# Performance work log

Hardware: AMD Instinct MI355X
Metric: run time of the kernel (lower is better)

Reference implementation:

```python
import jax, jax.numpy as jnp
import numpy as np
from jax import lax

B, C, H, W, K = 32, 128, 56, 56, 5
CR = C // 4          # reduced channels in weight-gen MLP
CE = 4 * C           # expanded channels
EPS = 1e-6


def setup_inputs() -> dict:
    key = jax.random.key(0)
    ks = jax.random.split(key, 8)
    s = lambda fan: 1.0 / np.sqrt(fan)
    return {
        "x": jax.random.normal(ks[0], (B, C, H, W), jnp.float32),
        "w_fc1": jax.random.normal(ks[1], (CR, C), jnp.float32) * s(C),
        "ln1_w": jnp.ones((CR,), jnp.float32),
        "ln1_b": jnp.zeros((CR,), jnp.float32),
        "w_fc2": jax.random.normal(ks[2], (C * K * K, CR), jnp.float32) * s(CR),
        "ln2_w": jnp.ones((C,), jnp.float32),
        "ln2_b": jnp.zeros((C,), jnp.float32),
        "w_expand": jax.random.normal(ks[3], (CE, C), jnp.float32) * s(C),
        "w_shrink": jax.random.normal(ks[4], (C, CE), jnp.float32) * s(CE),
        "grn_gamma": jax.random.normal(ks[5], (CE,), jnp.float32) * 0.1,
        "grn_beta": jax.random.normal(ks[6], (CE,), jnp.float32) * 0.1,
    }


def _ln(v, w, b, axis):
    u = v.mean(axis, keepdims=True)
    s2 = jnp.square(v - u).mean(axis, keepdims=True)
    return (v - u) * lax.rsqrt(s2 + EPS) * w + b


def reference(x, w_fc1, ln1_w, ln1_b, w_fc2, ln2_w, ln2_b, w_expand, w_shrink,
              grn_gamma, grn_beta):
    b, c, h, w = x.shape
    # ---- dynamic weight generation: pool -> fc1 -> LN -> fc2 ----
    pooled = x.mean((2, 3))                                  # [B, C]
    hdn = pooled @ w_fc1.T                                   # [B, CR]
    hdn = _ln(hdn, ln1_w, ln1_b, axis=-1)                    # channels_first LN over CR
    dyn = hdn @ w_fc2.T                                      # [B, C*K*K]
    dyn_w = dyn.reshape(b * c, 1, K, K)                      # per-sample depthwise kernels
    # ---- per-sample dynamic depthwise conv (groups = B*C) ----
    pad = K // 2
    out = lax.conv_general_dilated(
        x.reshape(1, b * c, h, w), dyn_w,
        window_strides=(1, 1), padding=[(pad, pad), (pad, pad)],
        dimension_numbers=("NCHW", "OIHW", "NCHW"),
        feature_group_count=b * c,
    ).reshape(b, c, h, w)
    # ---- LN (channels_first) over channel dim ----
    u = out.mean(1, keepdims=True)
    s2 = jnp.square(out - u).mean(1, keepdims=True)
    out = (out - u) * lax.rsqrt(s2 + EPS)
    out = ln2_w[None, :, None, None] * out + ln2_b[None, :, None, None]
    # ---- expand 1x1 -> GELU -> GRN -> shrink 1x1 ----
    out = jnp.einsum("bchw,oc->bohw", out, w_expand)         # [B, 4C, H, W]
    out = jax.nn.gelu(out, approximate=False)
    gx = jnp.sqrt(jnp.sum(jnp.square(out), axis=(2, 3), keepdims=True))  # [B,4C,1,1]
    nx = gx / (gx.mean(1, keepdims=True) + EPS)
    g = grn_gamma[None, :, None, None]
    bt = grn_beta[None, :, None, None]
    out = g * (out * nx) + bt + out
    out = jnp.einsum("bohw,co->bchw", out, w_shrink)         # [B, C, H, W]
    return out + x
```

## Files before the change

### kernel.cpp

```cpp
#include <hip/hip_runtime.h>
#include <hip/hip_bf16.h>

#define B_   32
#define C_   128
#define H_   56
#define W_   56
#define HW_  (H_*W_)
#define BHW_ (B_*HW_)
#define K5_  5
#define KK_  25
#define CR_  32
#define CE_  512
#define EPS_ 1e-6f

typedef __hip_bfloat16 bf16;
typedef __attribute__((ext_vector_type(8))) short short8;
typedef __attribute__((ext_vector_type(4))) float f32x4;


__device__ __forceinline__ float wave_reduce_sum(float v) {
#pragma unroll
  for (int off = 32; off > 0; off >>= 1) v += __shfl_down(v, off, 64);
  return v;
}
__device__ __forceinline__ float bf2f(unsigned short u) {
  return __uint_as_float(((unsigned)u) << 16);
}
__device__ __forceinline__ unsigned short f2bf_bits(float f) {
  bf16 h = __float2bfloat16(f);
  unsigned short u;
  __builtin_memcpy(&u, &h, 2);
  return u;
}
__device__ __forceinline__ float fast_gelu(float v) {
  float t = __expf(-1.702f * v);
  return v * __builtin_amdgcn_rcpf(1.0f + t);
}
__device__ __forceinline__ void glds16(const void* g, void* l) {
  __builtin_amdgcn_global_load_lds(
      (const __attribute__((address_space(1))) unsigned int*)g,
      (__attribute__((address_space(3))) unsigned int*)l, 16, 0, 0);
}

__global__ __launch_bounds__(256) void prep_kernel(const float* __restrict__ we,
                                                   const float* __restrict__ ws,
                                                   bf16* __restrict__ weB,
                                                   bf16* __restrict__ wsB,
                                                   float* __restrict__ gx2) {
  int i = blockIdx.x * 256 + threadIdx.x;
  if (i < CE_ * C_)          weB[i] = __float2bfloat16(we[i]);
  else if (i < 2 * CE_ * C_) wsB[i - CE_ * C_] = __float2bfloat16(ws[i - CE_ * C_]);
  else                       gx2[i - 2 * CE_ * C_] = 0.f;
}

__global__ __launch_bounds__(256) void pool_kernel(const float* __restrict__ x,
                                                   float* __restrict__ pooled) {
  int bc = blockIdx.x;
  const float4* xp4 = reinterpret_cast<const float4*>(x + (size_t)bc * HW_);
  float s = 0.f;
  for (int i = threadIdx.x; i < 784; i += 256) {
    float4 v = xp4[i];
    s += (v.x + v.y) + (v.z + v.w);
  }
  s = wave_reduce_sum(s);
  __shared__ float red[4];
  int lane = threadIdx.x & 63, wid = threadIdx.x >> 6;
  if (lane == 0) red[wid] = s;
  __syncthreads();
  if (threadIdx.x == 0) pooled[bc] = (red[0] + red[1] + red[2] + red[3]) * (1.0f / HW_);
}

__global__ __launch_bounds__(256) void fc_kernel(const float* __restrict__ pooled,
                                                 const float* __restrict__ w_fc1,
                                                 const float* __restrict__ ln1_w,
                                                 const float* __restrict__ ln1_b,
                                                 const float* __restrict__ w_fc2,
                                                 float* __restrict__ dyn) {
  int b = blockIdx.x;
  int tid = threadIdx.x;
  __shared__ float sp[C_];
  __shared__ float sh[CR_];
  __shared__ float shn[CR_];
  __shared__ float stats[2];
  if (tid < C_) sp[tid] = pooled[b * C_ + tid];
  __syncthreads();
  if (tid < CR_) {
    float acc = 0.f;
    const float* wr = w_fc1 + tid * C_;
#pragma unroll 4
    for (int c = 0; c < C_; ++c) acc += sp[c] * wr[c];
    sh[tid] = acc;
  }
  __syncthreads();
  if (tid == 0) {
    float u = 0.f;
    for (int j = 0; j < CR_; ++j) u += sh[j];
    u *= (1.0f / CR_);
    float v = 0.f;
    for (int j = 0; j < CR_; ++j) { float d = sh[j] - u; v += d * d; }
    v *= (1.0f / CR_);
    stats[0] = u;
    stats[1] = rsqrtf(v + EPS_);
  }
  __syncthreads();
  if (tid < CR_) shn[tid] = (sh[tid] - stats[0]) * stats[1] * ln1_w[tid] + ln1_b[tid];
  __syncthreads();
  for (int i = tid; i < C_ * KK_; i += 256) {
    const float* wr = w_fc2 + i * CR_;
    float acc = 0.f;
#pragma unroll
    for (int j = 0; j < CR_; ++j) acc += shn[j] * wr[j];
    dyn[b * (C_ * KK_) + i] = acc;
  }
}

__global__ __launch_bounds__(256) void conv_kernel(const float* __restrict__ x,
                                                   const float* __restrict__ dyn,
                                                   bf16* __restrict__ z) {
  int bc = blockIdx.x;
  int b = bc >> 7;
  int c = bc & 127;
  int tid = threadIdx.x;
  __shared__ float xs[(H_ + 4) * 64];
  __shared__ float wks[KK_];
  {
    int r = tid >> 6;
    int rr = (r < 2) ? r : (56 + r);
    xs[rr * 64 + (tid & 63)] = 0.f;
  }
  if (tid < 224) {
    int r = tid >> 2, q = tid & 3;
    int col = (q < 2) ? q : (56 + q);
    xs[(r + 2) * 64 + col] = 0.f;
  }
  if (tid < KK_) wks[tid] = dyn[b * (C_ * KK_) + c * KK_ + tid];
  const float4* xp4 = reinterpret_cast<const float4*>(x + (size_t)bc * HW_);
  for (int i = tid; i < 784; i += 256) {
    float4 v = xp4[i];
    int h = i / 14, w4 = (i % 14) * 4;
    float* dst = &xs[(h + 2) * 64 + 2 + w4];
    dst[0] = v.x; dst[1] = v.y; dst[2] = v.z; dst[3] = v.w;
  }
  __syncthreads();
  float wr[KK_];
#pragma unroll
  for (int j = 0; j < KK_; ++j) wr[j] = wks[j];
  for (int g = tid; g < 784; g += 256) {
    int h = g / 14;
    int w4 = (g % 14) * 4;
    float a0 = 0.f, a1 = 0.f, a2 = 0.f, a3 = 0.f;
#pragma unroll
    for (int dh = 0; dh < K5_; ++dh) {
      const float* row = &xs[(h + dh) * 64 + w4];
      float4 va = *reinterpret_cast<const float4*>(row);
      float4 vb = *reinterpret_cast<const float4*>(row + 4);
      float v0 = va.x, v1 = va.y, v2 = va.z, v3 = va.w;
      float v4 = vb.x, v5 = vb.y, v6 = vb.z, v7 = vb.w;
      float u0 = wr[dh * 5 + 0], u1 = wr[dh * 5 + 1], u2 = wr[dh * 5 + 2];
      float u3 = wr[dh * 5 + 3], u4 = wr[dh * 5 + 4];
      a0 += v0 * u0 + v1 * u1 + v2 * u2 + v3 * u3 + v4 * u4;
      a1 += v1 * u0 + v2 * u1 + v3 * u2 + v4 * u3 + v5 * u4;
      a2 += v2 * u0 + v3 * u1 + v4 * u2 + v5 * u3 + v6 * u4;
      a3 += v3 * u0 + v4 * u1 + v5 * u2 + v6 * u3 + v7 * u4;
    }
    size_t base = (size_t)bc * HW_ + h * W_ + w4;
    ushort4 pk = make_ushort4(f2bf_bits(a0), f2bf_bits(a1), f2bf_bits(a2), f2bf_bits(a3));
    *reinterpret_cast<ushort4*>(reinterpret_cast<unsigned short*>(z) + base) = pk;
  }
}

__global__ __launch_bounds__(256) void ln_kernel(const bf16* __restrict__ z,
                                                 const float* __restrict__ ln2_w,
                                                 const float* __restrict__ ln2_b,
                                                 bf16* __restrict__ yT) {
  int hw0 = blockIdx.x * 64;
  int b = blockIdx.y;
  int tid = threadIdx.x;
  int wq = tid & 63;
  int cq = tid >> 6;
  __shared__ unsigned short zt[C_][64];
  __shared__ unsigned short yt[64][136];
  __shared__ float redS[4][64];
  __shared__ float redQ[4][64];
  __shared__ float meanArr[64];
  __shared__ float invArr[64];
  float s = 0.f, q = 0.f;
  const unsigned short* zp = reinterpret_cast<const unsigned short*>(z);
#pragma unroll 4
  for (int k = 0; k < 32; ++k) {
    int c = cq * 32 + k;
    unsigned short u = zp[((size_t)(b * C_ + c)) * HW_ + hw0 + wq];
    float v = bf2f(u);
    s += v;
    q += v * v;
    zt[c][wq] = u;
  }
  redS[cq][wq] = s;
  redQ[cq][wq] = q;
  __syncthreads();
  if (cq == 0) {
    float ss = redS[0][wq] + redS[1][wq] + redS[2][wq] + redS[3][wq];
    float qq = redQ[0][wq] + redQ[1][wq] + redQ[2][wq] + redQ[3][wq];
    float m = ss * (1.0f / C_);
    float var = qq * (1.0f / C_) - m * m;
    meanArr[wq] = m;
    invArr[wq] = rsqrtf(fmaxf(var, 0.f) + EPS_);
  }
  __syncthreads();
  float m = meanArr[wq], iv = invArr[wq];
#pragma unroll
  for (int g = 0; g < 4; ++g) {
    unsigned short pk[8];
#pragma unroll
    for (int i = 0; i < 8; ++i) {
      int c = cq * 32 + g * 8 + i;
      float v = bf2f(zt[c][wq]);
      pk[i] = f2bf_bits((v - m) * iv * ln2_w[c] + ln2_b[c]);
    }
    int4 t;
    __builtin_memcpy(&t, pk, 16);
    *reinterpret_cast<int4*>(&yt[wq][cq * 32 + g * 8]) = t;
  }
  __syncthreads();
  unsigned short* yp = reinterpret_cast<unsigned short*>(yT);
#pragma unroll
  for (int i = 0; i < 4; ++i) {
    int t = tid + 256 * i;
    int row = t >> 4, ch = t & 15;
    int4 v = *reinterpret_cast<const int4*>(&yt[row][ch * 8]);
    *reinterpret_cast<int4*>(yp + ((size_t)(b * HW_ + hw0 + row)) * C_ + ch * 8) = v;
  }
}

__global__ __launch_bounds__(256, 4) void expand_mfma(const bf16* __restrict__ yT,
                                                      const bf16* __restrict__ weB,
                                                      bf16* __restrict__ eT,
                                                      float* __restrict__ gx2) {
  int j0 = blockIdx.x * 128;
  int o0 = blockIdx.y * 128;
  int tid = threadIdx.x;
  int lane = tid & 63, wid = tid >> 6;
  int wm = wid >> 1, wn = wid & 1;
  int quad = lane >> 4, l15 = lane & 15;
  __shared__ __align__(16) char smem[34816];
  const short* yS = reinterpret_cast<const short*>(yT);
  const short* weS = reinterpret_cast<const short*>(weB);
  int sr = (wid * 2) * 16 + (lane >> 2);
  int scp = lane & 3;
  auto STAGE = [&](int bs, int k0) {
#pragma unroll
    for (int i = 0; i < 2; ++i) {
      int seg = wid * 2 + i;
      int r = sr + i * 16;
      int c = scp ^ ((r >> 1) & 3);
      char* base = smem + bs * 16384 + seg * 1024;
      glds16(yS + (size_t)(j0 + r) * C_ + k0 + c * 8, base);
      glds16(weS + (size_t)(o0 + r) * C_ + k0 + c * 8, base + 8192);
    }
  };
  f32x4 acc[4][4] = {};
  STAGE(0, 0);
  __syncthreads();
#pragma unroll
  for (int t = 0; t < 4; ++t) {
    if (t < 3) STAGE((t + 1) & 1, (t + 1) * 32);
    const char* ba = smem + (t & 1) * 16384;
    int sx = (quad ^ ((l15 >> 1) & 3)) * 16;
    short8 a[4], bfr[4];
#pragma unroll
    for (int mf = 0; mf < 4; ++mf)
      a[mf] = *reinterpret_cast<const short8*>(ba + (wm * 64 + mf * 16 + l15) * 64 + sx);
#pragma unroll
    for (int nf = 0; nf < 4; ++nf)
      bfr[nf] = *reinterpret_cast<const short8*>(ba + 8192 + (wn * 64 + nf * 16 + l15) * 64 + sx);
#pragma unroll
    for (int mf = 0; mf < 4; ++mf)
#pragma unroll
      for (int nf = 0; nf < 4; ++nf)
        acc[mf][nf] = __builtin_amdgcn_mfma_f32_16x16x32_bf16(a[mf], bfr[nf], acc[mf][nf], 0, 0, 0);
    __syncthreads();
  }
  short (*Es)[136] = reinterpret_cast<short(*)[136]>(&smem[0]);
#pragma unroll
  for (int mf = 0; mf < 4; ++mf) {
    int jm = j0 + wm * 64 + mf * 16;
    int bb = jm / HW_;
    int jrow = wm * 64 + mf * 16 + quad * 4;
#pragma unroll
    for (int nf = 0; nf < 4; ++nf) {
      int oc = wn * 64 + nf * 16 + l15;
      float g2 = 0.f;
#pragma unroll
      for (int r = 0; r < 4; ++r) {
        float ge = fast_gelu(acc[mf][nf][r]);
        g2 += ge * ge;
        Es[jrow + r][oc] = (short)f2bf_bits(ge);
      }
      g2 += __shfl_xor(g2, 16, 64);
      g2 += __shfl_xor(g2, 32, 64);
      if (quad == 0) atomicAdd(&gx2[bb * CE_ + o0 + oc], g2);
    }
  }
  __syncthreads();
  unsigned short* eP = reinterpret_cast<unsigned short*>(eT);
#pragma unroll
  for (int i = 0; i < 8; ++i) {
    int t = tid + 256 * i;
    int row = t >> 4, ch = t & 15;
    int4 v = *reinterpret_cast<const int4*>(&Es[row][ch * 8]);
    *reinterpret_cast<int4*>(eP + (size_t)(j0 + row) * CE_ + o0 + ch * 8) = v;
  }
}

__global__ __launch_bounds__(512) void grn_scale_kernel(const float* __restrict__ gx2,
                                                        const float* __restrict__ gamma,
                                                        float* __restrict__ scale) {
  int b = blockIdx.x;
  int o = threadIdx.x;
  float gx = sqrtf(gx2[b * CE_ + o]);
  float s = wave_reduce_sum(gx);
  __shared__ float red[8];
  __shared__ float meansh;
  int lane = o & 63, wid = o >> 6;
  if (lane == 0) red[wid] = s;
  __syncthreads();
  if (o == 0) {
    float t = 0.f;
    for (int i = 0; i < 8; ++i) t += red[i];
    meansh = t * (1.0f / CE_);
  }
  __syncthreads();
  scale[b * CE_ + o] = 1.0f + gamma[o] * (gx / (meansh + EPS_));
}

__global__ __launch_bounds__(256) void sb_kernel(const float* __restrict__ w_shrink,
                                                 const float* __restrict__ beta,
                                                 float* __restrict__ sb) {
  int c = blockIdx.x;
  const float* wp = w_shrink + (size_t)c * CE_;
  float acc = 0.f;
  for (int o = threadIdx.x; o < CE_; o += 256) acc += wp[o] * beta[o];
  acc = wave_reduce_sum(acc);
  __shared__ float red[4];
  int lane = threadIdx.x & 63, wid = threadIdx.x >> 6;
  if (lane == 0) red[wid] = acc;
  __syncthreads();
  if (threadIdx.x == 0) sb[c] = red[0] + red[1] + red[2] + red[3];
}

__global__ __launch_bounds__(256) void scale_ws_kernel(const float* __restrict__ ws,
                                                       const float* __restrict__ scale,
                                                       bf16* __restrict__ sws) {
  int c = blockIdx.x;
  int b = blockIdx.y;
  const float* sp = scale + b * CE_;
  const float* wp = ws + (size_t)c * CE_;
  bf16* op = sws + ((size_t)(b * C_ + c)) * CE_;
  for (int i = threadIdx.x; i < CE_; i += 256)
    op[i] = __float2bfloat16(wp[i] * sp[i]);
}

__global__ __launch_bounds__(256, 2) void shrink_mfma(const bf16* __restrict__ eT,
                                                      const bf16* __restrict__ sws,
                                                      const float* __restrict__ sb,
                                                      const float* __restrict__ x,
                                                      float* __restrict__ out) {
  int hw0 = blockIdx.x * 128;
  int b = blockIdx.y;
  int tid = threadIdx.x;
  int lane = tid & 63, wid = tid >> 6;
  int wm = wid >> 1, wn = wid & 1;
  int quad = lane >> 4, l15 = lane & 15;
  __shared__ __align__(16) char smem[65536];
  const short* eS  = reinterpret_cast<const short*>(eT) + (size_t)b * HW_ * CE_;
  const short* wsS = reinterpret_cast<const short*>(sws) + (size_t)b * C_ * CE_;
  int sr0 = (wid * 4) * 8 + (lane >> 3);
  int scp = lane & 7;
  auto STAGE = [&](int bs, int k0) {
#pragma unroll
    for (int i = 0; i < 4; ++i) {
      int seg = wid * 4 + i;
      int r = sr0 + i * 8;
      int c = scp ^ (r & 7);
      int hwc = hw0 + r; if (hwc >= HW_) hwc = HW_ - 1;
      char* base = smem + bs * 32768 + seg * 1024;
      glds16(eS + (size_t)hwc * CE_ + k0 + c * 8, base);
      glds16(wsS + (size_t)r * CE_ + k0 + c * 8, base + 16384);
    }
  };
  f32x4 acc[4][4] = {};
  STAGE(0, 0);
  __syncthreads();
#pragma unroll 1
  for (int t = 0; t < 8; ++t) {
    if (t < 7) STAGE((t + 1) & 1, (t + 1) * 64);
    const char* ba = smem + (t & 1) * 32768;
#pragma unroll
    for (int ks = 0; ks < 2; ++ks) {
      short8 a[4], bfr[4];
#pragma unroll
      for (int mf = 0; mf < 4; ++mf) {
        int cp = (ks * 4 + quad) ^ (l15 & 7);
        a[mf] = *reinterpret_cast<const short8*>(ba + (wm * 64 + mf * 16 + l15) * 128 + cp * 16);
      }
#pragma unroll
      for (int nf = 0; nf < 4; ++nf) {
        int cp = (ks * 4 + quad) ^ (l15 & 7);
        bfr[nf] = *reinterpret_cast<const short8*>(ba + 16384 + (wn * 64 + nf * 16 + l15) * 128 + cp * 16);
      }
#pragma unroll
      for (int mf = 0; mf < 4; ++mf)
#pragma unroll
        for (int nf = 0; nf < 4; ++nf)
          acc[mf][nf] = __builtin_amdgcn_mfma_f32_16x16x32_bf16(a[mf], bfr[nf], acc[mf][nf], 0, 0, 0);
    }
    __syncthreads();
  }
  float (*Ef)[132] = reinterpret_cast<float(*)[132]>(&smem[0]);
#pragma unroll 1
  for (int phase = 0; phase < 2; ++phase) {
    if (wn == phase) {
#pragma unroll
      for (int mf = 0; mf < 4; ++mf) {
        int hwr = wm * 64 + mf * 16 + quad * 4;
#pragma unroll
        for (int nf = 0; nf < 4; ++nf)
          *reinterpret_cast<f32x4*>(&Ef[nf * 16 + l15][hwr]) = acc[mf][nf];
      }
    }
    __syncthreads();
#pragma unroll
    for (int i = 0; i < 8; ++i) {
      int t = tid + 256 * i;
      int row = t >> 5, ch = t & 31;
      int hw = hw0 + ch * 4;
      if (hw < HW_) {
        int c = phase * 64 + row;
        size_t base = ((size_t)(b * C_ + c)) * HW_ + hw;
        float add = sb[c];
        f32x4 av = *reinterpret_cast<const f32x4*>(&Ef[row][ch * 4]);
        float4 xv = *reinterpret_cast<const float4*>(x + base);
        float4 ov;
        ov.x = av.x + add + xv.x;
        ov.y = av.y + add + xv.y;
        ov.z = av.z + add + xv.z;
        ov.w = av.w + add + xv.w;
        *reinterpret_cast<float4*>(out + base) = ov;
      }
    }
    __syncthreads();
  }
}

extern "C" void kernel_launch(void* const* d_in, const int* in_sizes, int n_in,
                              void* d_out, int out_size, void* d_ws, size_t ws_size,
                              hipStream_t stream) {
  (void)in_sizes; (void)n_in; (void)out_size; (void)ws_size;
  const float* x        = (const float*)d_in[0];
  const float* w_fc1    = (const float*)d_in[1];
  const float* ln1_w    = (const float*)d_in[2];
  const float* ln1_b    = (const float*)d_in[3];
  const float* w_fc2    = (const float*)d_in[4];
  const float* ln2_w    = (const float*)d_in[5];
  const float* ln2_b    = (const float*)d_in[6];
  const float* w_expand = (const float*)d_in[7];
  const float* w_shrink = (const float*)d_in[8];
  const float* gamma    = (const float*)d_in[9];
  const float* beta     = (const float*)d_in[10];
  float* out = (float*)d_out;

  char* ws = (char*)d_ws;
  float* pooled = (float*)(ws + 0);
  float* dyn    = (float*)(ws + 16384);
  float* gx2    = (float*)(ws + 425984);
  float* scale  = (float*)(ws + 491520);
  float* sb     = (float*)(ws + 557056);
  bf16*  weB    = (bf16*)(ws + 557568);
  bf16*  wsB    = (bf16*)(ws + 688640);
  bf16*  yT     = (bf16*)(ws + 819712);
  bf16*  sws    = (bf16*)(ws + 819712);
  bf16*  eT     = (bf16*)(ws + 26509824);
  bf16*  z      = eT;

  prep_kernel<<<576, 256, 0, stream>>>(w_expand, w_shrink, weB, wsB, gx2);
  sb_kernel<<<C_, 256, 0, stream>>>(w_shrink, beta, sb);
  pool_kernel<<<B_ * C_, 256, 0, stream>>>(x, pooled);
  fc_kernel<<<B_, 256, 0, stream>>>(pooled, w_fc1, ln1_w, ln1_b, w_fc2, dyn);
  conv_kernel<<<B_ * C_, 256, 0, stream>>>(x, dyn, z);
  ln_kernel<<<dim3(49, B_), 256, 0, stream>>>(z, ln2_w, ln2_b, yT);
  expand_mfma<<<dim3(784, 4), 256, 0, stream>>>(yT, weB, eT, gx2);
  grn_scale_kernel<<<B_, 512, 0, stream>>>(gx2, gamma, scale);
  scale_ws_kernel<<<dim3(C_, B_), 256, 0, stream>>>(w_shrink, scale, sws);
  shrink_mfma<<<dim3(25, B_), 256, 0, stream>>>(eT, sws, sb, x, out);
}
```

Before: 266.6 us.

## Halve shrink GEMM tile to 64 pixels and vectorize LN kernel loads

The shrink MFMA kernel moves from 128-pixel tiles to 64-pixel tiles. With 3136 = 49×64, this drops the edge clamping and bounds checks, raises the grid from 800 to 1568 blocks, and cuts shared memory so three blocks can fit per CU. The epilogue becomes a single pass instead of two phases. The LN kernel now loads z with 16-byte vector loads into shared memory first and reduces from there, replacing scalar 2-byte global loads. The cost is that each sws weight tile is reloaded by twice as many blocks, and LN gains an extra barrier.

```diff
diff --git a/kernel.cpp b/kernel.cpp
--- a/kernel.cpp
+++ b/kernel.cpp
@@ -184,16 +184,21 @@
   __shared__ float redQ[4][64];
   __shared__ float meanArr[64];
   __shared__ float invArr[64];
+  const unsigned short* zp = reinterpret_cast<const unsigned short*>(z);
+#pragma unroll
+  for (int i = 0; i < 4; ++i) {
+    int t = tid + 256 * i;
+    int c = t >> 3, ch = t & 7;
+    int4 v = *reinterpret_cast<const int4*>(zp + ((size_t)(b * C_ + c)) * HW_ + hw0 + ch * 8);
+    *reinterpret_cast<int4*>(&zt[c][ch * 8]) = v;
+  }
+  __syncthreads();
   float s = 0.f, q = 0.f;
-  const unsigned short* zp = reinterpret_cast<const unsigned short*>(z);
 #pragma unroll 4
   for (int k = 0; k < 32; ++k) {
-    int c = cq * 32 + k;
-    unsigned short u = zp[((size_t)(b * C_ + c)) * HW_ + hw0 + wq];
-    float v = bf2f(u);
+    float v = bf2f(zt[cq * 32 + k][wq]);
     s += v;
     q += v * v;
-    zt[c][wq] = u;
   }
   redS[cq][wq] = s;
   redQ[cq][wq] = q;
@@ -360,95 +365,93 @@
     op[i] = __float2bfloat16(wp[i] * sp[i]);
 }
 
-__global__ __launch_bounds__(256, 2) void shrink_mfma(const bf16* __restrict__ eT,
+__global__ __launch_bounds__(256, 3) void shrink_mfma(const bf16* __restrict__ eT,
                                                       const bf16* __restrict__ sws,
                                                       const float* __restrict__ sb,
                                                       const float* __restrict__ x,
                                                       float* __restrict__ out) {
-  int hw0 = blockIdx.x * 128;
+  int hw0 = blockIdx.x * 64;
   int b = blockIdx.y;
   int tid = threadIdx.x;
   int lane = tid & 63, wid = tid >> 6;
   int wm = wid >> 1, wn = wid & 1;
   int quad = lane >> 4, l15 = lane & 15;
-  __shared__ __align__(16) char smem[65536];
+  __shared__ __align__(16) char smem[49152];
   const short* eS  = reinterpret_cast<const short*>(eT) + (size_t)b * HW_ * CE_;
   const short* wsS = reinterpret_cast<const short*>(sws) + (size_t)b * C_ * CE_;
-  int sr0 = (wid * 4) * 8 + (lane >> 3);
-  int scp = lane & 7;
+  int lr = lane >> 3;
+  int lc = lane & 7;
   auto STAGE = [&](int bs, int k0) {
+    char* base = smem + bs * 24576;
+#pragma unroll
+    for (int i = 0; i < 2; ++i) {
+      int seg = wid * 2 + i;
+      int r = seg * 8 + lr;
+      int c = lc ^ (r & 7);
+      glds16(eS + (size_t)(hw0 + r) * CE_ + k0 + c * 8, base + seg * 1024);
+    }
 #pragma unroll
     for (int i = 0; i < 4; ++i) {
       int seg = wid * 4 + i;
-      int r = sr0 + i * 8;
-      int c = scp ^ (r & 7);
-      int hwc = hw0 + r; if (hwc >= HW_) hwc = HW_ - 1;
-      char* base = smem + bs * 32768 + seg * 1024;
-      glds16(eS + (size_t)hwc * CE_ + k0 + c * 8, base);
-      glds16(wsS + (size_t)r * CE_ + k0 + c * 8, base + 16384);
+      int r = seg * 8 + lr;
+      int c = lc ^ (r & 7);
+      glds16(wsS + (size_t)r * CE_ + k0 + c * 8, base + 8192 + seg * 1024);
     }
   };
-  f32x4 acc[4][4] = {};
+  f32x4 acc[2][4] = {};
   STAGE(0, 0);
   __syncthreads();
 #pragma unroll 1
   for (int t = 0; t < 8; ++t) {
     if (t < 7) STAGE((t + 1) & 1, (t + 1) * 64);
-    const char* ba = smem + (t & 1) * 32768;
+    const char* ba = smem + (t & 1) * 24576;
 #pragma unroll
     for (int ks = 0; ks < 2; ++ks) {
-      short8 a[4], bfr[4];
-#pragma unroll
-      for (int mf = 0; mf < 4; ++mf) {
-        int cp = (ks * 4 + quad) ^ (l15 & 7);
-        a[mf] = *reinterpret_cast<const short8*>(ba + (wm * 64 + mf * 16 + l15) * 128 + cp * 16);
+      short8 a[2], bfr[4];
+#pragma unroll
+      for (int mf = 0; mf < 2; ++mf) {
+        int row = wm * 32 + mf * 16 + l15;
+        int cp = (ks * 4 + quad) ^ (row & 7);
+        a[mf] = *reinterpret_cast<const short8*>(ba + row * 128 + cp * 16);
       }
 #pragma unroll
       for (int nf = 0; nf < 4; ++nf) {
-        int cp = (ks * 4 + quad) ^ (l15 & 7);
-        bfr[nf] = *reinterpret_cast<const short8*>(ba + 16384 + (wn * 64 + nf * 16 + l15) * 128 + cp * 16);
+        int row = wn * 64 + nf * 16 + l15;
+        int cp = (ks * 4 + quad) ^ (row & 7);
+        bfr[nf] = *reinterpret_cast<const short8*>(ba + 8192 + row * 128 + cp * 16);
       }
 #pragma unroll
-      for (int mf = 0; mf < 4; ++mf)
+      for (int mf = 0; mf < 2; ++mf)
 #pragma unroll
         for (int nf = 0; nf < 4; ++nf)
           acc[mf][nf] = __builtin_amdgcn_mfma_f32_16x16x32_bf16(a[mf], bfr[nf], acc[mf][nf], 0, 0, 0);
     }
     __syncthreads();
   }
-  float (*Ef)[132] = reinterpret_cast<float(*)[132]>(&smem[0]);
-#pragma unroll 1
-  for (int phase = 0; phase < 2; ++phase) {
-    if (wn == phase) {
-#pragma unroll
-      for (int mf = 0; mf < 4; ++mf) {
-        int hwr = wm * 64 + mf * 16 + quad * 4;
-#pragma unroll
-        for (int nf = 0; nf < 4; ++nf)
-          *reinterpret_cast<f32x4*>(&Ef[nf * 16 + l15][hwr]) = acc[mf][nf];
-      }
-    }
-    __syncthreads();
-#pragma unroll
-    for (int i = 0; i < 8; ++i) {
-      int t = tid + 256 * i;
-      int row = t >> 5, ch = t & 31;
-      int hw = hw0 + ch * 4;
-      if (hw < HW_) {
-        int c = phase * 64 + row;
-        size_t base = ((size_t)(b * C_ + c)) * HW_ + hw;
-        float add = sb[c];
-        f32x4 av = *reinterpret_cast<const f32x4*>(&Ef[row][ch * 4]);
-        float4 xv = *reinterpret_cast<const float4*>(x + base);
-        float4 ov;
-        ov.x = av.x + add + xv.x;
-        ov.y = av.y + add + xv.y;
-        ov.z = av.z + add + xv.z;
-        ov.w = av.w + add + xv.w;
-        *reinterpret_cast<float4*>(out + base) = ov;
-      }
-    }
-    __syncthreads();
+  float (*Ef)[68] = reinterpret_cast<float(*)[68]>(&smem[0]);
+#pragma unroll
+  for (int mf = 0; mf < 2; ++mf) {
+    int hwr = wm * 32 + mf * 16 + quad * 4;
+#pragma unroll
+    for (int nf = 0; nf < 4; ++nf)
+      *reinterpret_cast<f32x4*>(&Ef[wn * 64 + nf * 16 + l15][hwr]) = acc[mf][nf];
+  }
+  __syncthreads();
+#pragma unroll
+  for (int i = 0; i < 8; ++i) {
+    int t = tid + 256 * i;
+    int row = t >> 4, ch = t & 15;
+    int hw = hw0 + ch * 4;
+    size_t base = ((size_t)(b * C_ + row)) * HW_ + hw;
+    float add = sb[row];
+    f32x4 av = *reinterpret_cast<const f32x4*>(&Ef[row][ch * 4]);
+    float4 xv = *reinterpret_cast<const float4*>(x + base);
+    float4 ov;
+    ov.x = av.x + add + xv.x;
+    ov.y = av.y + add + xv.y;
+    ov.z = av.z + add + xv.z;
+    ov.w = av.w + add + xv.w;
+    *reinterpret_cast<float4*>(out + base) = ov;
   }
 }
 
@@ -491,5 +494,5 @@
   expand_mfma<<<dim3(784, 4), 256, 0, stream>>>(yT, weB, eT, gx2);
   grn_scale_kernel<<<B_, 512, 0, stream>>>(gx2, gamma, scale);
   scale_ws_kernel<<<dim3(C_, B_), 256, 0, stream>>>(w_shrink, scale, sws);
-  shrink_mfma<<<dim3(25, B_), 256, 0, stream>>>(eT, sws, sb, x, out);
-}
+  shrink_mfma<<<dim3(49, B_), 256, 0, stream>>>(eT, sws, sb, x, out);
+}
```

New measurement: 264.3 us. About the same (-0.9%).
